# Optimization experiments

Measured on AMD Instinct MI355X. Metric: run time of the kernel, lower is better.

## Reference

```python
import jax, jax.numpy as jnp
import numpy as np
from jax import lax

INPUT_SIZE = 512
STRIDES = (8, 16, 32)
NUM_CLASSES = 2
KA = 3  # anchors per scale
EPS = 1e-8
ANCHORS = np.array([[[10, 13], [16, 30], [33, 23]],
                    [[30, 61], [62, 45], [59, 119]],
                    [[116, 90], [156, 198], [373, 326]]], dtype=np.float32)

def _grid(stride):
    f = INPUT_SIZE // stride
    gy, gx = np.meshgrid(np.arange(f), np.arange(f), indexing='ij')
    return jnp.asarray(np.stack([gx, gy], -1).reshape(-1, 2).astype(np.float32))  # [HW,2] (x,y)

GRIDS = [_grid(s) for s in STRIDES]


def conv_ltc(x, conv_w, bn_gamma, bn_beta, cm, vleak, tau_m, e_revin):
    """Discrete LTC recurrence over time (tau_input=True, usetaum=True, stream_opt=True).
    x: [B,T,C,H,W] -> [B,T,Cout,H,W]"""
    B, T, C, H, W = x.shape
    Cout = conv_w.shape[0]

    def step(v_pre, xt):
        z = lax.conv_general_dilated(xt, conv_w, (1, 1), ((1, 1), (1, 1)),
                                     dimension_numbers=('NCHW', 'OIHW', 'NCHW'))
        wih = z * bn_gamma + bn_beta  # BatchNorm in eval form (per-channel affine)
        num = tau_m * v_pre / (vleak + cm * jax.nn.sigmoid(wih)) + wih * e_revin
        v = jax.nn.sigmoid(num / (1.0 + EPS))
        return v, v

    v0 = jnp.zeros((B, Cout, H, W), x.dtype)
    _, ys = lax.scan(step, v0, jnp.moveaxis(x, 1, 0))  # [T,B,Cout,H,W]
    return jnp.moveaxis(ys, 0, 1)


def head(y, w, b):
    # 1x1 conv detection head
    return jnp.einsum('bchw,oc->bohw', y, w) + b[None, :, None, None]


def decode_scale(pred, i):
    """pred: [B, KA*(1+C+4), h, w] -> obj [B,hw*KA,1], cls [B,hw*KA,C], box [B,hw*KA,4]."""
    B, _, h, w = pred.shape
    s = STRIDES[i]
    p = jnp.transpose(pred, (0, 2, 3, 1))  # [B,h,w,21]
    obj = p[..., :KA].reshape(B, -1, 1)
    cls = p[..., KA:KA * (1 + NUM_CLASSES)].reshape(B, -1, NUM_CLASSES)
    reg = p[..., KA * (1 + NUM_CLASSES):].reshape(B, h * w, KA, 4)
    anchors = jnp.asarray(ANCHORS[i])  # [KA,2]
    xy = (jax.nn.sigmoid(reg[..., :2]) + GRIDS[i][None, :, None, :]) * s
    wh = jnp.exp(reg[..., 2:]) * anchors[None, None, :, :]
    xywh = jnp.concatenate([xy, wh], -1).reshape(B, -1, 4)
    box = jnp.concatenate([xywh[..., :2] - xywh[..., 2:] * 0.5,
                           xywh[..., :2] + xywh[..., 2:] * 0.5], -1) / INPUT_SIZE
    return obj, cls, box


def setup_inputs() -> dict:
    key = jax.random.key(0)
    ks = jax.random.split(key, 12)
    B = 8
    x = jax.random.uniform(ks[0], (B, 5, 5, 512, 512), jnp.float32)
    y1 = jax.random.normal(ks[1], (B, 768, 16, 16), jnp.float32)
    y2 = jax.random.normal(ks[2], (B, 384, 32, 32), jnp.float32)
    y3 = jax.random.normal(ks[3], (B, 192, 64, 64), jnp.float32)
    conv_w = jax.random.normal(ks[4], (5, 5, 3, 3), jnp.float32) * 0.15  # xavier-ish
    bn_gamma = jnp.ones((5, 1, 1), jnp.float32)
    bn_beta = jnp.zeros((5, 1, 1), jnp.float32)
    cm = 1.0 + 0.1 * jax.random.normal(ks[5], (5, 1, 1), jnp.float32)
    vleak = 1.0 + 0.1 * jax.random.normal(ks[6], (5, 1, 1), jnp.float32)
    tau_m = 0.8 - 0.3 * jax.random.uniform(ks[7], (5, 1, 1), jnp.float32)
    e_revin = 1.0 + 0.1 * jax.random.normal(ks[8], (5, 1, 1), jnp.float32)
    OC = KA * (1 + NUM_CLASSES + 4)  # 21
    w1 = jax.random.normal(ks[9], (OC, 768), jnp.float32) * 0.02
    w2 = jax.random.normal(ks[10], (OC, 384), jnp.float32) * 0.02
    w3 = jax.random.normal(ks[11], (OC, 192), jnp.float32) * 0.02
    b1 = jnp.zeros((OC,), jnp.float32)
    b2 = jnp.zeros((OC,), jnp.float32)
    b3 = jnp.zeros((OC,), jnp.float32)
    return dict(x=x, y1=y1, y2=y2, y3=y3, conv_w=conv_w, bn_gamma=bn_gamma,
                bn_beta=bn_beta, cm=cm, vleak=vleak, tau_m=tau_m, e_revin=e_revin,
                w1=w1, b1=b1, w2=w2, b2=b2, w3=w3, b3=b3)


def reference(x, y1, y2, y3, conv_w, bn_gamma, bn_beta, cm, vleak, tau_m, e_revin,
              w1, b1, w2, b2, w3, b3):
    enc = conv_ltc(x, conv_w, bn_gamma, bn_beta, cm, vleak, tau_m, e_revin)
    # preds ordered [pred_s (y3, stride 8), pred_m (y2, 16), pred_l (y1, 32)]
    preds = [head(y3, w3, b3), head(y2, w2, b2), head(y1, w1, b1)]
    objs, clss, boxes = [], [], []
    for i, p in enumerate(preds):
        o, c, bx = decode_scale(p, i)
        objs.append(o); clss.append(c); boxes.append(bx)
    det = jnp.concatenate([jnp.concatenate(objs, 1),
                           jnp.concatenate(clss, 1),
                           jnp.concatenate(boxes, 1)], -1)  # [B, 16128, 7]
    return enc, det
```

## Files before the change

kernel.cpp:

```cpp
#include <hip/hip_runtime.h>
#include <math.h>

#define HH 512
#define WW 512
#define HWp (HH * WW)
#define TT 5
#define CC 5

#define CTW 64
#define CTH 16
#define NROW (CTH + 2)
#define GCOL 18
#define LCP (GCOL * 4)
#define LDSF (CC * NROW * LCP)
#define NG (CC * NROW * GCOL)
#define NBUF 2
#define SPARE_BYTES (NBUF * LDSF * 4)

#define NHEADB 672
#define NCONVB 2048

#define LDS_TOTAL (NBUF * LDSF + 256)

typedef float v2f __attribute__((ext_vector_type(2)));

typedef __attribute__((address_space(3))) char       lds_char_t;
typedef __attribute__((address_space(1)))  const char glb_char_t;

__device__ __forceinline__ float fast_sigmoid(float x) {
    return __builtin_amdgcn_rcpf(1.0f + __expf(-x));
}

extern "C" __global__ __launch_bounds__(512, 4)
void spikefpn_fused(const float* __restrict__ x, const float* __restrict__ cw,
                    const float* __restrict__ gamma, const float* __restrict__ beta,
                    const float* __restrict__ cm, const float* __restrict__ vleak,
                    const float* __restrict__ tau, const float* __restrict__ erev,
                    const float* __restrict__ y3, const float* __restrict__ w3, const float* __restrict__ b3,
                    const float* __restrict__ y2, const float* __restrict__ w2, const float* __restrict__ b2,
                    const float* __restrict__ y1, const float* __restrict__ w1, const float* __restrict__ b1,
                    float* __restrict__ out, float* __restrict__ det)
{
    __shared__ float xs[LDS_TOTAL];

    const int bid = blockIdx.x;
    const int tid = threadIdx.x;

    if (bid < NHEADB) {
        float* smem = xs;
        const float *y, *w, *bias;
        int Cin, f, lgf, lgchunks, row_off;
        float s;
        float aw0, aw1, aw2, ah0, ah1, ah2;
        int sb;

        if (bid < 512) {
            sb = bid;       y = y3; w = w3; bias = b3; Cin = 192; f = 64; lgf = 6; lgchunks = 6; s = 8.0f;  row_off = 0;
            aw0 = 10.f;  ah0 = 13.f;  aw1 = 16.f;  ah1 = 30.f;  aw2 = 33.f;  ah2 = 23.f;
        } else if (bid < 640) {
            sb = bid - 512; y = y2; w = w2; bias = b2; Cin = 384; f = 32; lgf = 5; lgchunks = 4; s = 16.0f; row_off = 12288;
            aw0 = 30.f;  ah0 = 61.f;  aw1 = 62.f;  ah1 = 45.f;  aw2 = 59.f;  ah2 = 119.f;
        } else {
            sb = bid - 640; y = y1; w = w1; bias = b1; Cin = 768; f = 16; lgf = 4; lgchunks = 2; s = 32.0f; row_off = 15360;
            aw0 = 116.f; ah0 = 90.f;  aw1 = 156.f; ah1 = 198.f; aw2 = 373.f; ah2 = 326.f;
        }

        const int n     = f * f;
        const int b     = sb >> lgchunks;
        const int chunk = sb & ((1 << lgchunks) - 1);

        const int lane = tid & 63;
        const int grp  = tid >> 6;
        const int pix  = (chunk << 6) + lane;

        const int nhalf = (Cin >= 768) ? 2 : 1;
        const int Chalf = Cin / nhalf;
        const int G     = Chalf >> 3;

        float acc[21];
        #pragma unroll
        for (int o = 0; o < 21; ++o) acc[o] = 0.0f;

        for (int h = 0; h < nhalf; ++h) {
            const int wtot = Chalf * 21;
            for (int i = tid; i < wtot; i += 512) {
                int o = i / Chalf;
                int c = i - o * Chalf;
                smem[c * 24 + o] = w[o * Cin + h * Chalf + c];
            }
            __syncthreads();

            const float* yp = y + ((size_t)b * Cin + (size_t)(h * Chalf + grp * G)) * n + pix;
            const int wbase = grp * G * 24;

            #pragma unroll 4
            for (int c = 0; c < G; ++c) {
                float v = yp[(size_t)c * n];
                const float* wr = &smem[wbase + c * 24];
                float4 q0 = *(const float4*)(wr);
                float4 q1 = *(const float4*)(wr + 4);
                float4 q2 = *(const float4*)(wr + 8);
                float4 q3 = *(const float4*)(wr + 12);
                float4 q4 = *(const float4*)(wr + 16);
                float  s20 = wr[20];
                float wv[21] = {q0.x,q0.y,q0.z,q0.w, q1.x,q1.y,q1.z,q1.w,
                                q2.x,q2.y,q2.z,q2.w, q3.x,q3.y,q3.z,q3.w,
                                q4.x,q4.y,q4.z,q4.w, s20};
                #pragma unroll
                for (int o = 0; o < 21; ++o) acc[o] = fmaf(v, wv[o], acc[o]);
            }
            __syncthreads();
        }

        #pragma unroll
        for (int o = 0; o < 21; ++o) smem[tid * 21 + o] = acc[o];
        __syncthreads();

        if (tid < 64) {
            float r[21];
            #pragma unroll
            for (int o = 0; o < 21; ++o) r[o] = bias[o];
            #pragma unroll
            for (int g2 = 0; g2 < 8; ++g2) {
                const float* rp = &smem[(g2 * 64 + lane) * 21];
                #pragma unroll
                for (int o = 0; o < 21; ++o) r[o] += rp[o];
            }

            const int hy = pix >> lgf;
            const int hx = pix & (f - 1);
            const float inv = 1.0f / 512.0f;
            const float AW[3] = {aw0, aw1, aw2};
            const float AH[3] = {ah0, ah1, ah2};

            #pragma unroll
            for (int a = 0; a < 3; ++a) {
                const int row = row_off + pix * 3 + a;
                float* dp = det + ((size_t)b * 16128 + row) * 7;
                dp[0] = r[a];
                dp[1] = r[3 + a * 2];
                dp[2] = r[4 + a * 2];
                float cx = (fast_sigmoid(r[9  + a * 4]) + (float)hx) * s;
                float cy = (fast_sigmoid(r[10 + a * 4]) + (float)hy) * s;
                float bw = __expf(r[11 + a * 4]) * AW[a];
                float bh = __expf(r[12 + a * 4]) * AH[a];
                dp[3] = (cx - bw * 0.5f) * inv;
                dp[4] = (cy - bh * 0.5f) * inv;
                dp[5] = (cx + bw * 0.5f) * inv;
                dp[6] = (cy + bh * 0.5f) * inv;
            }
        }
        return;
    }

    const int cb = bid - NHEADB;
    const int bx = cb & 7;
    const int by = (cb >> 3) & 31;
    const int b  = cb >> 8;

    const int grow0 = by * CTH;
    const int gcol0 = bx * CTW;
    const size_t xb = (size_t)b * (TT * CC * HWp);

    int  goff[4];
    bool pred[4];
    uint32_t gbase[4];
    #pragma unroll
    for (int k = 0; k < 4; ++k) {
        const int g = tid + k * 512;
        const int wavebase = (tid & ~63) + k * 512;
        if (wavebase >= NG) {
            pred[k] = true;
            goff[k] = 0;
            gbase[k] = (uint32_t)SPARE_BYTES;
        } else {
            const bool valid = g < NG;
            const int gg  = valid ? g : 0;
            const int ch  = gg / (NROW * GCOL);
            const int rem = gg - ch * (NROW * GCOL);
            const int row = rem / GCOL;
            const int c4  = rem - row * GCOL;
            const int gr = grow0 + row - 1;
            const int gc = gcol0 - 4 + c4 * 4;
            const bool inb = valid && ((unsigned)gr < (unsigned)HH) && ((unsigned)gc < (unsigned)WW);
            pred[k] = inb;
            goff[k] = ch * HWp + gr * WW + gc;
            gbase[k] = (uint32_t)(wavebase * 16);
            if (valid && !inb) {
                float4 z = make_float4(0.f, 0.f, 0.f, 0.f);
                *(float4*)&xs[g * 4]        = z;
                *(float4*)&xs[LDSF + g * 4] = z;
            }
        }
    }

    lds_char_t* lds0 = (lds_char_t*)xs;

    auto issue_stage = [&](int t, int buf) {
        const float* xt = x + xb + (size_t)t * (CC * HWp);
        const uint32_t bufoff = (uint32_t)buf * (LDSF * 4);
        #pragma unroll
        for (int k = 0; k < 4; ++k) {
            if (pred[k]) {
                __builtin_amdgcn_global_load_lds(
                    (const __attribute__((address_space(1))) void*)(glb_char_t*)(const char*)(xt + goff[k]),
                    (__attribute__((address_space(3))) void*)(lds0 + bufoff + gbase[k]),
                    16, 0, 0);
            }
        }
    };

    float g_[CC], be[CC], cmv[CC], vl[CC], tm[CC], er[CC];
    #pragma unroll
    for (int o = 0; o < CC; ++o) {
        g_[o] = gamma[o]; be[o] = beta[o]; cmv[o] = cm[o];
        vl[o] = vleak[o]; tm[o] = tau[o]; er[o] = erev[o];
    }

    const int tx = tid & 63;
    const int r0 = (tid >> 6) * 2;

    issue_stage(0, 0);
    asm volatile("s_waitcnt vmcnt(0)" ::: "memory");
    asm volatile("s_waitcnt lgkmcnt(0)" ::: "memory");
    __builtin_amdgcn_s_barrier();
    __builtin_amdgcn_sched_barrier(0);

    v2f vpre[CC];
    #pragma unroll
    for (int o = 0; o < CC; ++o) vpre[o] = (v2f){0.0f, 0.0f};

    #pragma unroll
    for (int t = 0; t < TT; ++t) {
        if (t + 1 < TT) issue_stage(t + 1, (t + 1) & 1);

        const float* cur = xs + (t & 1) * LDSF;

        v2f acc[CC];
        #pragma unroll
        for (int o = 0; o < CC; ++o) acc[o] = (v2f){0.0f, 0.0f};

        #pragma unroll
        for (int ic = 0; ic < CC; ++ic) {
            const float* lp = &cur[(ic * NROW + r0) * LCP + tx + 3];
            v2f xv[3][3];
            #pragma unroll
            for (int dr = 0; dr < 3; ++dr)
                #pragma unroll
                for (int dc = 0; dc < 3; ++dc)
                    xv[dr][dc] = (v2f){lp[dr * LCP + dc], lp[(dr + 1) * LCP + dc]};
            #pragma unroll
            for (int oc = 0; oc < CC; ++oc) {
                const float* wp = cw + (oc * CC + ic) * 9;
                v2f a = acc[oc];
                #pragma unroll
                for (int dr = 0; dr < 3; ++dr)
                    #pragma unroll
                    for (int dc = 0; dc < 3; ++dc) {
                        const float w = wp[dr * 3 + dc];
                        a = __builtin_elementwise_fma((v2f){w, w}, xv[dr][dc], a);
                    }
                acc[oc] = a;
            }
        }

        const size_t ob0 = (size_t)(grow0 + r0) * WW + gcol0 + tx;
        #pragma unroll
        for (int o = 0; o < CC; ++o) {
            float* op = out + ((size_t)((b * TT + t) * CC + o)) * HWp + ob0;

            float wih0 = fmaf(acc[o].x, g_[o], be[o]);
            float sg0  = fast_sigmoid(wih0);
            float den0 = fmaf(cmv[o], sg0, vl[o]);
            float num0 = fmaf(tm[o] * vpre[o].x, __builtin_amdgcn_rcpf(den0), wih0 * er[o]);
            float v0   = fast_sigmoid(num0);
            vpre[o].x = v0;
            op[0] = v0;

            float wih1 = fmaf(acc[o].y, g_[o], be[o]);
            float sg1  = fast_sigmoid(wih1);
            float den1 = fmaf(cmv[o], sg1, vl[o]);
            float num1 = fmaf(tm[o] * vpre[o].y, __builtin_amdgcn_rcpf(den1), wih1 * er[o]);
            float v1   = fast_sigmoid(num1);
            vpre[o].y = v1;
            op[WW] = v1;
        }

        if (t < TT - 1) {
            asm volatile("s_waitcnt vmcnt(10)" ::: "memory");
            __builtin_amdgcn_s_barrier();
            __builtin_amdgcn_sched_barrier(0);
        }
    }
}

extern "C" void kernel_launch(void* const* d_in, const int* in_sizes, int n_in,
                              void* d_out, int out_size, void* d_ws, size_t ws_size,
                              hipStream_t stream)
{
    const float* x     = (const float*)d_in[0];
    const float* y1    = (const float*)d_in[1];
    const float* y2    = (const float*)d_in[2];
    const float* y3    = (const float*)d_in[3];
    const float* cw    = (const float*)d_in[4];
    const float* gamma = (const float*)d_in[5];
    const float* beta  = (const float*)d_in[6];
    const float* cm    = (const float*)d_in[7];
    const float* vleak = (const float*)d_in[8];
    const float* tau   = (const float*)d_in[9];
    const float* erev  = (const float*)d_in[10];
    const float* w1    = (const float*)d_in[11];
    const float* b1    = (const float*)d_in[12];
    const float* w2    = (const float*)d_in[13];
    const float* b2    = (const float*)d_in[14];
    const float* w3    = (const float*)d_in[15];
    const float* b3    = (const float*)d_in[16];

    float* out = (float*)d_out;
    float* det = out + (size_t)8 * TT * CC * HH * WW;

    spikefpn_fused<<<dim3(NHEADB + NCONVB), 512, 0, stream>>>(
        x, cw, gamma, beta, cm, vleak, tau, erev,
        y3, w3, b3, y2, w2, b2, y1, w1, b1, out, det);
}
```

Measured before the change: 143.6 us.

## Triple-buffer LTC input stages, repack conv weights, fold log2e into sigmoids

```diff
diff --git a/kernel.cpp b/kernel.cpp
--- a/kernel.cpp
+++ b/kernel.cpp
@@ -14,7 +14,7 @@
 #define LCP (GCOL * 4)
 #define LDSF (CC * NROW * LCP)
 #define NG (CC * NROW * GCOL)
-#define NBUF 2
+#define NBUF 3
 #define SPARE_BYTES (NBUF * LDSF * 4)
 
 #define NHEADB 672
@@ -31,8 +31,19 @@
     return __builtin_amdgcn_rcpf(1.0f + __expf(-x));
 }
 
+extern "C" __global__ void repack_w_kernel(const float* __restrict__ cw, float* __restrict__ wr) {
+    const int i = threadIdx.x;
+    if (i < 300) {
+        const int k  = i % 12;
+        const int p  = i / 12;
+        const int ic = p / 5;
+        const int oc = p - ic * 5;
+        wr[i] = (k < 9) ? cw[(oc * 5 + ic) * 9 + k] : 0.0f;
+    }
+}
+
 extern "C" __global__ __launch_bounds__(512, 4)
-void spikefpn_fused(const float* __restrict__ x, const float* __restrict__ cw,
+void spikefpn_fused(const float* __restrict__ x, const float* __restrict__ wr,
                     const float* __restrict__ gamma, const float* __restrict__ beta,
                     const float* __restrict__ cm, const float* __restrict__ vleak,
                     const float* __restrict__ tau, const float* __restrict__ erev,
@@ -96,13 +107,13 @@
             #pragma unroll 4
             for (int c = 0; c < G; ++c) {
                 float v = yp[(size_t)c * n];
-                const float* wr = &smem[wbase + c * 24];
-                float4 q0 = *(const float4*)(wr);
-                float4 q1 = *(const float4*)(wr + 4);
-                float4 q2 = *(const float4*)(wr + 8);
-                float4 q3 = *(const float4*)(wr + 12);
-                float4 q4 = *(const float4*)(wr + 16);
-                float  s20 = wr[20];
+                const float* wrr = &smem[wbase + c * 24];
+                float4 q0 = *(const float4*)(wrr);
+                float4 q1 = *(const float4*)(wrr + 4);
+                float4 q2 = *(const float4*)(wrr + 8);
+                float4 q3 = *(const float4*)(wrr + 12);
+                float4 q4 = *(const float4*)(wrr + 16);
+                float  s20 = wrr[20];
                 float wv[21] = {q0.x,q0.y,q0.z,q0.w, q1.x,q1.y,q1.z,q1.w,
                                 q2.x,q2.y,q2.z,q2.w, q3.x,q3.y,q3.z,q3.w,
                                 q4.x,q4.y,q4.z,q4.w, s20};
@@ -188,8 +199,9 @@
             gbase[k] = (uint32_t)(wavebase * 16);
             if (valid && !inb) {
                 float4 z = make_float4(0.f, 0.f, 0.f, 0.f);
-                *(float4*)&xs[g * 4]        = z;
-                *(float4*)&xs[LDSF + g * 4] = z;
+                *(float4*)&xs[g * 4]            = z;
+                *(float4*)&xs[LDSF + g * 4]     = z;
+                *(float4*)&xs[2 * LDSF + g * 4] = z;
             }
         }
     }
@@ -210,18 +222,28 @@
         }
     };
 
-    float g_[CC], be[CC], cmv[CC], vl[CC], tm[CC], er[CC];
+    const float L2E = 1.442695040888963f;
+    v2f g2[CC], be2[CC], cmv2[CC], vl2[CC], gL2[CC], bL2[CC], tmL2[CC], erL2[CC];
     #pragma unroll
     for (int o = 0; o < CC; ++o) {
-        g_[o] = gamma[o]; be[o] = beta[o]; cmv[o] = cm[o];
-        vl[o] = vleak[o]; tm[o] = tau[o]; er[o] = erev[o];
+        float g = gamma[o], be = beta[o], cmo = cm[o], vlo = vleak[o];
+        float tmo = tau[o], ero = erev[o];
+        g2[o]   = (v2f){g, g};
+        be2[o]  = (v2f){be, be};
+        cmv2[o] = (v2f){cmo, cmo};
+        vl2[o]  = (v2f){vlo, vlo};
+        gL2[o]  = (v2f){-g * L2E, -g * L2E};
+        bL2[o]  = (v2f){-be * L2E, -be * L2E};
+        tmL2[o] = (v2f){-tmo * L2E, -tmo * L2E};
+        erL2[o] = (v2f){-ero * L2E, -ero * L2E};
     }
 
     const int tx = tid & 63;
     const int r0 = (tid >> 6) * 2;
 
     issue_stage(0, 0);
-    asm volatile("s_waitcnt vmcnt(0)" ::: "memory");
+    issue_stage(1, 1);
+    asm volatile("s_waitcnt vmcnt(4)" ::: "memory");
     asm volatile("s_waitcnt lgkmcnt(0)" ::: "memory");
     __builtin_amdgcn_s_barrier();
     __builtin_amdgcn_sched_barrier(0);
@@ -232,9 +254,9 @@
 
     #pragma unroll
     for (int t = 0; t < TT; ++t) {
-        if (t + 1 < TT) issue_stage(t + 1, (t + 1) & 1);
-
-        const float* cur = xs + (t & 1) * LDSF;
+        if (t + 2 < TT) issue_stage(t + 2, (t + 2) % NBUF);
+
+        const float* cur = xs + (t % NBUF) * LDSF;
 
         v2f acc[CC];
         #pragma unroll
@@ -249,9 +271,10 @@
                 #pragma unroll
                 for (int dc = 0; dc < 3; ++dc)
                     xv[dr][dc] = (v2f){lp[dr * LCP + dc], lp[(dr + 1) * LCP + dc]};
+            const float* wic = wr + ic * 60;
             #pragma unroll
             for (int oc = 0; oc < CC; ++oc) {
-                const float* wp = cw + (oc * CC + ic) * 9;
+                const float* wp = wic + oc * 12;
                 v2f a = acc[oc];
                 #pragma unroll
                 for (int dr = 0; dr < 3; ++dr)
@@ -269,24 +292,30 @@
         for (int o = 0; o < CC; ++o) {
             float* op = out + ((size_t)((b * TT + t) * CC + o)) * HWp + ob0;
 
-            float wih0 = fmaf(acc[o].x, g_[o], be[o]);
-            float sg0  = fast_sigmoid(wih0);
-            float den0 = fmaf(cmv[o], sg0, vl[o]);
-            float num0 = fmaf(tm[o] * vpre[o].x, __builtin_amdgcn_rcpf(den0), wih0 * er[o]);
-            float v0   = fast_sigmoid(num0);
-            vpre[o].x = v0;
-            op[0] = v0;
-
-            float wih1 = fmaf(acc[o].y, g_[o], be[o]);
-            float sg1  = fast_sigmoid(wih1);
-            float den1 = fmaf(cmv[o], sg1, vl[o]);
-            float num1 = fmaf(tm[o] * vpre[o].y, __builtin_amdgcn_rcpf(den1), wih1 * er[o]);
-            float v1   = fast_sigmoid(num1);
-            vpre[o].y = v1;
+            v2f a    = acc[o];
+            v2f wih  = __builtin_elementwise_fma(a, g2[o], be2[o]);
+            v2f targ = __builtin_elementwise_fma(a, gL2[o], bL2[o]);
+            float sg0 = __builtin_amdgcn_rcpf(1.0f + __builtin_amdgcn_exp2f(targ.x));
+            float sg1 = __builtin_amdgcn_rcpf(1.0f + __builtin_amdgcn_exp2f(targ.y));
+            v2f den  = __builtin_elementwise_fma((v2f){sg0, sg1}, cmv2[o], vl2[o]);
+            float rd0 = __builtin_amdgcn_rcpf(den.x);
+            float rd1 = __builtin_amdgcn_rcpf(den.y);
+            v2f tv = vpre[o] * tmL2[o];
+            v2f we = wih * erL2[o];
+            float n0 = fmaf(tv.x, rd0, we.x);
+            float n1 = fmaf(tv.y, rd1, we.y);
+            float v0 = __builtin_amdgcn_rcpf(1.0f + __builtin_amdgcn_exp2f(n0));
+            float v1 = __builtin_amdgcn_rcpf(1.0f + __builtin_amdgcn_exp2f(n1));
+            vpre[o] = (v2f){v0, v1};
+            op[0]  = v0;
             op[WW] = v1;
         }
 
-        if (t < TT - 1) {
+        if (t <= 2) {
+            asm volatile("s_waitcnt vmcnt(14)" ::: "memory");
+            __builtin_amdgcn_s_barrier();
+            __builtin_amdgcn_sched_barrier(0);
+        } else if (t == 3) {
             asm volatile("s_waitcnt vmcnt(10)" ::: "memory");
             __builtin_amdgcn_s_barrier();
             __builtin_amdgcn_sched_barrier(0);
@@ -318,8 +347,11 @@
 
     float* out = (float*)d_out;
     float* det = out + (size_t)8 * TT * CC * HH * WW;
+    float* wrs = (float*)d_ws;
+
+    repack_w_kernel<<<dim3(1), 512, 0, stream>>>(cw, wrs);
 
     spikefpn_fused<<<dim3(NHEADB + NCONVB), 512, 0, stream>>>(
-        x, cw, gamma, beta, cm, vleak, tau, erev,
+        x, wrs, gamma, beta, cm, vleak, tau, erev,
         y3, w3, b3, y2, w2, b2, y1, w1, b1, out, det);
 }
```

Result: slower. 152.2 us (+6.0%).
